# Kernel tuning notes

Measured on AMD Instinct MI355X. Metric: run time of the kernel, lower is better.

## Reference

```python
import jax, jax.numpy as jnp
import numpy as np
import math

B, Q_LEN, PAST, HID = 1, 1024, 3072, 4096
NH, NKV, HD = 32, 8, 128
KV_LEN = PAST + Q_LEN
ROPE_THETA = 10000.0


def setup_inputs() -> dict:
    key = jax.random.key(0)
    ks = jax.random.split(key, 8)
    s = 0.02
    hidden_states = jax.random.normal(ks[0], (B, Q_LEN, HID), jnp.float32)
    # additive causal mask with KV cache offset: query i attends keys j <= PAST + i
    i = jnp.arange(Q_LEN)[:, None]
    j = jnp.arange(KV_LEN)[None, :]
    attention_mask = jnp.where(j <= PAST + i, 0.0, -1e9).astype(jnp.float32)[None, None]
    position_ids = (jnp.arange(Q_LEN, dtype=jnp.int64) + PAST)[None, :]
    past_k = jax.random.normal(ks[1], (B, NKV, PAST, HD), jnp.float32)
    past_v = jax.random.normal(ks[2], (B, NKV, PAST, HD), jnp.float32)
    Wq = jax.random.normal(ks[3], (NH * HD, HID), jnp.float32) * s
    Wk = jax.random.normal(ks[4], (NKV * HD, HID), jnp.float32) * s
    Wv = jax.random.normal(ks[5], (NKV * HD, HID), jnp.float32) * s
    Wo = jax.random.normal(ks[6], (HID, NH * HD), jnp.float32) * s
    return {"hidden_states": hidden_states, "attention_mask": attention_mask,
            "position_ids": position_ids, "past_k": past_k, "past_v": past_v,
            "Wq": Wq, "Wk": Wk, "Wv": Wv, "Wo": Wo}


def _rope_tables(seq_len, head_dim, dtype):
    inv_freq = 1.0 / (ROPE_THETA ** (jnp.arange(0, head_dim, 2, dtype=jnp.float32) / head_dim))
    t = jnp.arange(seq_len, dtype=jnp.float32)
    freqs = jnp.outer(t, inv_freq)            # [seq, hd/2]
    emb = jnp.concatenate([freqs, freqs], -1)  # [seq, hd]
    return jnp.cos(emb).astype(dtype), jnp.sin(emb).astype(dtype)


def _rotate_half(x):
    x1, x2 = jnp.split(x, 2, axis=-1)
    return jnp.concatenate([-x2, x1], axis=-1)


def reference(hidden_states, attention_mask, position_ids, past_k, past_v, Wq, Wk, Wv, Wo):
    bsz, q_len, _ = hidden_states.shape
    q = (hidden_states @ Wq.T).reshape(bsz, q_len, NH, HD).transpose(0, 2, 1, 3)
    k = (hidden_states @ Wk.T).reshape(bsz, q_len, NKV, HD).transpose(0, 2, 1, 3)
    v = (hidden_states @ Wv.T).reshape(bsz, q_len, NKV, HD).transpose(0, 2, 1, 3)

    kv_seq_len = q_len + past_k.shape[2]
    cos_t, sin_t = _rope_tables(kv_seq_len, HD, q.dtype)
    cos = cos_t[position_ids][:, None]  # [b,1,q,hd]
    sin = sin_t[position_ids][:, None]
    q = q * cos + _rotate_half(q) * sin
    k = k * cos + _rotate_half(k) * sin

    k = jnp.concatenate([past_k, k], axis=2)  # [b,nkv,kv,hd]
    v = jnp.concatenate([past_v, v], axis=2)
    n_rep = NH // NKV
    k = jnp.repeat(k, n_rep, axis=1)  # GQA repeat_kv -> [b,nh,kv,hd]
    v = jnp.repeat(v, n_rep, axis=1)

    scores = jnp.einsum('bhqd,bhkd->bhqk', q, k) / math.sqrt(HD)
    scores = scores + attention_mask
    weights = jax.nn.softmax(scores.astype(jnp.float32), axis=-1).astype(q.dtype)
    attn = jnp.einsum('bhqk,bhkd->bhqd', weights, v)
    attn = attn.transpose(0, 2, 1, 3).reshape(bsz, q_len, NH * HD)
    return attn @ Wo.T
```

## Files before the change

### kernel.cpp

```cpp
#include <hip/hip_runtime.h>

#define QLEN 1024
#define PASTN 3072
#define KVLEN 4096
#define HIDN 4096
#define NHEAD 32
#define NKVH 8
#define HDIM 128
#define NQKVC 6144
#define PLANE ((size_t)QLEN * NQKVC)

typedef unsigned short u16;
typedef __bf16 bf16x8 __attribute__((ext_vector_type(8)));
typedef float f32x4 __attribute__((ext_vector_type(4)));
typedef float f32x16 __attribute__((ext_vector_type(16)));
typedef u16 us8 __attribute__((ext_vector_type(8)));
typedef u16 us4 __attribute__((ext_vector_type(4)));

__device__ __forceinline__ u16 f2bf(float x) {
  unsigned u = __builtin_bit_cast(unsigned, x);
  u += 0x7fffu + ((u >> 16) & 1u);
  return (u16)(u >> 16);
}
__device__ __forceinline__ float bf2f(u16 b) {
  return __builtin_bit_cast(float, (unsigned)b << 16);
}

#define GLL16(gp, lp) __builtin_amdgcn_global_load_lds( \
    (const __attribute__((address_space(1))) void*)(gp), \
    (__attribute__((address_space(3))) void*)(lp), 16, 0, 0)

__global__ __launch_bounds__(256) void cvt5_kernel(const float* __restrict__ hid,
                                                   const float* __restrict__ wq,
                                                   const float* __restrict__ wk,
                                                   const float* __restrict__ wv,
                                                   const float* __restrict__ woin,
                                                   u16* __restrict__ hb,
                                                   u16* __restrict__ wb,
                                                   u16* __restrict__ wob) {
  const int blk = blockIdx.x;
  const float* src;
  u16* dst;
  int off;
  if (blk < 4096)       { src = hid;  dst = hb;                       off = blk; }
  else if (blk < 20480) { src = wq;   dst = wb;                       off = blk - 4096; }
  else if (blk < 24576) { src = wk;   dst = wb + (size_t)4096 * HIDN; off = blk - 20480; }
  else if (blk < 28672) { src = wv;   dst = wb + (size_t)5120 * HIDN; off = blk - 24576; }
  else                  { src = woin; dst = wob;                      off = blk - 28672; }
  const int i = off * 1024 + threadIdx.x * 4;
  float4 f = *(const float4*)(src + i);
  ushort4 o = make_ushort4(f2bf(f.x), f2bf(f.y), f2bf(f.z), f2bf(f.w));
  *(ushort4*)(dst + i) = o;
}

__global__ __launch_bounds__(256) void gemm_bt_split(const u16* __restrict__ A,
                                                     const u16* __restrict__ B,
                                                     float* __restrict__ P,
                                                     int M, int N, int K, int Ks) {
  __shared__ u16 Alds[2][64 * 32];
  __shared__ u16 Blds[2][128 * 32];
  const int tid = threadIdx.x, wid = tid >> 6, lane = tid & 63;
  const int m0 = blockIdx.y * 64, n0 = blockIdx.x * 128;
  const int z = blockIdx.z;
  const u16* Az = A + (size_t)z * Ks;
  const u16* Bz = B + (size_t)z * Ks;
  float* Cz = P + (size_t)z * M * N;
  const int wm = (wid >> 1) * 32, wn = (wid & 1) * 64;
  const int l15 = lane & 15, l4 = lane >> 4;
  const int srow = lane >> 2, sp = lane & 3;
  f32x4 acc[2][4] = {};
  auto stage = [&](int buf, int kt) {
    {
      const int r = wid * 16 + srow;
      GLL16(Az + (size_t)(m0 + r) * K + kt + (sp ^ ((r >> 1) & 3)) * 8,
            &Alds[buf][wid * 512]);
    }
#pragma unroll
    for (int i = 0; i < 2; ++i) {
      const int c = wid * 2 + i;
      const int r = c * 16 + srow;
      GLL16(Bz + (size_t)(n0 + r) * K + kt + (sp ^ ((r >> 1) & 3)) * 8,
            &Blds[buf][c * 512]);
    }
  };
  stage(0, 0);
  __syncthreads();
  int cur = 0;
  for (int kt = 0; kt < Ks; kt += 32) {
    if (kt + 32 < Ks) stage(cur ^ 1, kt + 32);
    bf16x8 a[2], b[4];
#pragma unroll
    for (int i = 0; i < 2; ++i) {
      const int R = wm + i * 16 + l15;
      a[i] = *(const bf16x8*)&Alds[cur][R * 32 + (l4 ^ ((R >> 1) & 3)) * 8];
    }
#pragma unroll
    for (int j = 0; j < 4; ++j) {
      const int R = wn + j * 16 + l15;
      b[j] = *(const bf16x8*)&Blds[cur][R * 32 + (l4 ^ ((R >> 1) & 3)) * 8];
    }
#pragma unroll
    for (int i = 0; i < 2; ++i)
#pragma unroll
      for (int j = 0; j < 4; ++j)
        acc[i][j] = __builtin_amdgcn_mfma_f32_16x16x32_bf16(a[i], b[j], acc[i][j], 0, 0, 0);
    __syncthreads();
    cur ^= 1;
  }
#pragma unroll
  for (int i = 0; i < 2; ++i)
#pragma unroll
    for (int j = 0; j < 4; ++j) {
      int row = m0 + wm + i * 16 + l4 * 4;
      int col = n0 + wn + j * 16 + l15;
#pragma unroll
      for (int r = 0; r < 4; ++r) Cz[(size_t)(row + r) * N + col] = acc[i][j][r];
    }
}

__global__ __launch_bounds__(256) void comb2_f32(const float* __restrict__ P,
                                                 float* __restrict__ C, size_t MN) {
  const size_t i = ((size_t)blockIdx.x * 256 + threadIdx.x) * 4;
  f32x4 a = *(const f32x4*)(P + i);
  f32x4 b = *(const f32x4*)(P + MN + i);
  f32x4 o;
#pragma unroll
  for (int j = 0; j < 4; ++j) o[j] = a[j] + b[j];
  *(f32x4*)(C + i) = o;
}

__global__ __launch_bounds__(256) void rope_q_kernel(const float* __restrict__ g,
                                                     u16* __restrict__ qr) {
  const float SC = 0.12753102f;
  int idx = blockIdx.x * 256 + threadIdx.x;
  int i = idx & 63, h = (idx >> 6) & 31, r = idx >> 11;
  float freq = __expf(-(float)i * (9.210340371976184f / 64.f));
  float angle = (float)(PASTN + r) * freq;
  float sn, cs;
  sincosf(angle, &sn, &cs);
  const size_t base = (size_t)r * NQKVC + h * HDIM + i;
  float x1 = g[base] + g[base + PLANE];
  float x2 = g[base + 64] + g[base + 64 + PLANE];
  int ob = r * HIDN + h * HDIM + i;
  qr[ob] = f2bf((x1 * cs - x2 * sn) * SC);
  qr[ob + 64] = f2bf((x2 * cs + x1 * sn) * SC);
}

__global__ __launch_bounds__(256) void repack_k_kernel(const float* __restrict__ past_k,
                                                       const float* __restrict__ g,
                                                       u16* __restrict__ kb) {
  int idx = blockIdx.x * 256 + threadIdx.x;
  int d = idx & 127, kv = (idx >> 7) & 4095, hk = idx >> 19;
  float val;
  if (kv < PASTN) {
    val = past_k[((size_t)hk * PASTN + kv) * HDIM + d];
  } else {
    int r = kv - PASTN;
    const size_t b0 = (size_t)r * NQKVC + 4096 + hk * HDIM;
    float x = g[b0 + d] + g[b0 + d + PLANE];
    float xp = g[b0 + (d ^ 64)] + g[b0 + (d ^ 64) + PLANE];
    int i = d & 63;
    float freq = __expf(-(float)i * (9.210340371976184f / 64.f));
    float angle = (float)(PASTN + r) * freq;
    float sn, cs;
    sincosf(angle, &sn, &cs);
    val = (d < 64) ? (x * cs - xp * sn) : (x * cs + xp * sn);
  }
  kb[idx] = f2bf(val);
}

__global__ __launch_bounds__(256) void repack_vt_kernel(const float* __restrict__ past_v,
                                                        const float* __restrict__ g,
                                                        u16* __restrict__ vtb) {
  __shared__ u16 tile[32][136];
  int hk = blockIdx.y, kv0 = blockIdx.x * 32, tid = threadIdx.x;
  int j = tid >> 3, d0 = (tid & 7) * 16;
  if (kv0 < PASTN) {
    const float* src = past_v + ((size_t)hk * PASTN + kv0 + j) * HDIM + d0;
#pragma unroll
    for (int x = 0; x < 16; x += 4) {
      float4 f = *(const float4*)(src + x);
      tile[j][d0 + x] = f2bf(f.x);
      tile[j][d0 + x + 1] = f2bf(f.y);
      tile[j][d0 + x + 2] = f2bf(f.z);
      tile[j][d0 + x + 3] = f2bf(f.w);
    }
  } else {
    int r = kv0 - PASTN + j;
    const float* s0 = g + (size_t)r * NQKVC + 5120 + hk * HDIM + d0;
#pragma unroll
    for (int x = 0; x < 16; x += 4) {
      f32x4 a = *(const f32x4*)(s0 + x);
      f32x4 b = *(const f32x4*)(s0 + PLANE + x);
#pragma unroll
      for (int jj = 0; jj < 4; ++jj) tile[j][d0 + x + jj] = f2bf(a[jj] + b[jj]);
    }
  }
  __syncthreads();
  int d = tid >> 1, jb = (tid & 1) * 16;
  us8 o0, o1;
#pragma unroll
  for (int x = 0; x < 8; ++x) {
    o0[x] = tile[jb + x][d];
    o1[x] = tile[jb + 8 + x][d];
  }
  u16* dst = vtb + ((size_t)hk * HDIM + d) * KVLEN + kv0 + jb;
  *(us8*)dst = o0;
  *(us8*)(dst + 8) = o1;
}

__global__ __launch_bounds__(512) void attn_kernel(const u16* __restrict__ q,
                                                   const u16* __restrict__ kc,
                                                   const u16* __restrict__ vt,
                                                   float* __restrict__ opart,
                                                   float* __restrict__ mlbuf) {
  __shared__ u16 Klds[2][64 * 128];
  __shared__ u16 Vlds[2][128 * 64];
  const int tid = threadIdx.x, wid = tid >> 6, lane = tid & 63;
  const int l31 = lane & 31, hi = lane >> 5, l15 = lane & 15;
  const int h = blockIdx.y, hk = h >> 2;
  const int q0 = blockIdx.x * 256;
  const int z = blockIdx.z;
  const int pid = h * 4 + blockIdx.x;
  const int qrow = q0 + wid * 32 + l31;
  bf16x8 qf[8];
  {
    const u16* qp = q + (size_t)qrow * HIDN + h * HDIM + hi * 8;
#pragma unroll
    for (int dk = 0; dk < 8; ++dk) qf[dk] = *(const bf16x8*)(qp + dk * 16);
  }
  float m_run = -1e30f, l_run = 0.f;
  f32x16 oacc[4] = {};
  const u16* kbase = kc + (size_t)hk * KVLEN * HDIM;
  const u16* vbase = vt + (size_t)hk * HDIM * KVLEN;
  const int ntiles = (PASTN + q0 + 256) >> 6;
  const int half = ntiles >> 1;
  const int t0 = z ? half : 0, t1 = z ? ntiles : half;
  const int qpos = PASTN + qrow;
  auto stage = [&](int buf, int kv0) {
#pragma unroll
    for (int i = 0; i < 2; ++i) {
      const int w = wid * 2 + i;
      const int p = w * 4 + (lane >> 4);
      const int key = (p & 0x33) | ((p & 4) << 1) | ((p & 8) >> 1);
      const int sl = (lane & 15) ^ (p & 15);
      GLL16(kbase + (size_t)(kv0 + key) * HDIM + sl * 8, &Klds[buf][w * 512]);
    }
#pragma unroll
    for (int i = 0; i < 2; ++i) {
      const int w = wid * 2 + i;
      const int d = w * 8 + (lane >> 3);
      const int sl = (lane & 7) ^ ((lane >> 3) & 7);
      GLL16(vbase + (size_t)d * KVLEN + kv0 + sl * 8, &Vlds[buf][w * 512]);
    }
  };
  stage(0, t0 << 6);
  __syncthreads();
  int cur = 0;
  for (int t = t0; t < t1; ++t) {
    if (t + 1 < t1) stage(cur ^ 1, (t + 1) << 6);
    const int kv0 = t << 6;
    const u16* Kb = Klds[cur];
    const u16* Vb = Vlds[cur];
    f32x16 s[2] = {};
    __builtin_amdgcn_s_setprio(1);
#pragma unroll
    for (int tt = 0; tt < 2; ++tt)
#pragma unroll
      for (int dk = 0; dk < 8; ++dk) {
        const int idx = (tt * 32 + l31) * 128 + (((dk * 2 + hi) ^ l15) * 8);
        bf16x8 kf = *(const bf16x8*)&Kb[idx];
        s[tt] = __builtin_amdgcn_mfma_f32_32x32x16_bf16(kf, qf[dk], s[tt], 0, 0, 0);
      }
    __builtin_amdgcn_s_setprio(0);
    float pm = -1e30f;
    if (kv0 + 63 > PASTN + q0) {
#pragma unroll
      for (int tt = 0; tt < 2; ++tt)
#pragma unroll
        for (int reg = 0; reg < 16; ++reg) {
          const int key = kv0 + tt * 32 + (reg & 7) + 8 * hi + ((reg & 8) << 1);
          float v = s[tt][reg];
          if (key > qpos) v = -1e30f;
          s[tt][reg] = v;
          pm = fmaxf(pm, v);
        }
    } else {
#pragma unroll
      for (int tt = 0; tt < 2; ++tt)
#pragma unroll
        for (int reg = 0; reg < 16; ++reg) pm = fmaxf(pm, s[tt][reg]);
    }
    pm = fmaxf(pm, __shfl_xor(pm, 32));
    if (!__all(pm <= m_run)) {
      const float mn = fmaxf(m_run, pm);
      const float corr = exp2f(m_run - mn);
      m_run = mn;
      l_run *= corr;
#pragma unroll
      for (int db = 0; db < 4; ++db)
#pragma unroll
        for (int r = 0; r < 16; ++r) oacc[db][r] *= corr;
    }
    float rs = 0.f;
#pragma unroll
    for (int tt = 0; tt < 2; ++tt)
#pragma unroll
      for (int reg = 0; reg < 16; ++reg) {
        const float p = exp2f(s[tt][reg] - m_run);
        s[tt][reg] = p;
        rs += p;
      }
    rs += __shfl_xor(rs, 32);
    l_run += rs;
    __builtin_amdgcn_s_setprio(1);
#pragma unroll
    for (int kc2 = 0; kc2 < 4; ++kc2) {
      bf16x8 pa;
#pragma unroll
      for (int j = 0; j < 8; ++j) pa[j] = (__bf16)s[kc2 >> 1][(kc2 & 1) * 8 + j];
#pragma unroll
      for (int db = 0; db < 4; ++db) {
        const int idx = (db * 32 + l31) * 64 + (((kc2 * 2 + hi) ^ (l31 & 7)) * 8);
        bf16x8 vf = *(const bf16x8*)&Vb[idx];
        oacc[db] = __builtin_amdgcn_mfma_f32_32x32x16_bf16(vf, pa, oacc[db], 0, 0, 0);
      }
    }
    __builtin_amdgcn_s_setprio(0);
    __syncthreads();
    cur ^= 1;
  }
  const int orow = wid * 32 + l31;
  float* op = opart + ((size_t)(z * 128 + pid) * 256 + orow) * 128;
#pragma unroll
  for (int db = 0; db < 4; ++db)
#pragma unroll
    for (int g = 0; g < 4; ++g) {
      f32x4 w4;
#pragma unroll
      for (int j = 0; j < 4; ++j) w4[j] = oacc[db][g * 4 + j];
      *(f32x4*)&op[db * 32 + g * 8 + hi * 4] = w4;
    }
  if (hi == 0) {
    float* mlp = mlbuf + ((size_t)(z * 128 + pid) * 256 + orow) * 2;
    mlp[0] = m_run;
    mlp[1] = l_run;
  }
}

__global__ __launch_bounds__(256) void attn_combine(const float* __restrict__ opart,
                                                    const float* __restrict__ mlbuf,
                                                    u16* __restrict__ o) {
  const int pid = blockIdx.x;
  const int h = pid >> 2, qt = pid & 3;
  const int q2 = threadIdx.x >> 2, dc = (threadIdx.x & 3) * 32;
#pragma unroll
  for (int b = 0; b < 4; ++b) {
    const int q = b * 64 + q2;
    const float* ml0 = mlbuf + ((size_t)pid * 256 + q) * 2;
    const float* ml1 = mlbuf + ((size_t)(128 + pid) * 256 + q) * 2;
    const float m0 = ml0[0], l0 = ml0[1], m1 = ml1[0], l1 = ml1[1];
    const float m = fmaxf(m0, m1);
    const float w0 = exp2f(m0 - m), w1 = exp2f(m1 - m);
    const float inv = 1.f / (w0 * l0 + w1 * l1);
    const float* O0 = opart + ((size_t)pid * 256 + q) * 128 + dc;
    const float* O1 = opart + ((size_t)(128 + pid) * 256 + q) * 128 + dc;
    u16* dst = o + (size_t)(qt * 256 + q) * HIDN + h * HDIM + dc;
#pragma unroll
    for (int x = 0; x < 8; ++x) {
      f32x4 a = *(const f32x4*)(O0 + x * 4);
      f32x4 bb = *(const f32x4*)(O1 + x * 4);
      us4 w4;
#pragma unroll
      for (int j = 0; j < 4; ++j) w4[j] = f2bf((a[j] * w0 + bb[j] * w1) * inv);
      *(us4*)(dst + x * 4) = w4;
    }
  }
}

extern "C" void kernel_launch(void* const* d_in, const int* in_sizes, int n_in,
                              void* d_out, int out_size, void* d_ws, size_t ws_size,
                              hipStream_t stream) {
  (void)in_sizes; (void)n_in; (void)out_size; (void)ws_size;
  const float* hidden = (const float*)d_in[0];
  const float* past_k = (const float*)d_in[3];
  const float* past_v = (const float*)d_in[4];
  const float* Wq = (const float*)d_in[5];
  const float* Wk = (const float*)d_in[6];
  const float* Wv = (const float*)d_in[7];
  const float* Wo = (const float*)d_in[8];
  float* out = (float*)d_out;

  char* w = (char*)d_ws;
  u16* hiddenb = (u16*)w; w += (size_t)QLEN * HIDN * 2;
  u16* wqkv    = (u16*)w; w += (size_t)NQKVC * HIDN * 2;
  u16* wo      = (u16*)w; w += (size_t)HIDN * HIDN * 2;
  u16* qrope   = (u16*)w; w += (size_t)QLEN * HIDN * 2;
  u16* kbuf    = (u16*)w; w += (size_t)NKVH * KVLEN * HDIM * 2;
  u16* vtbuf   = (u16*)w; w += (size_t)NKVH * HDIM * KVLEN * 2;
  u16* attnb   = (u16*)w; w += (size_t)QLEN * HIDN * 2;
  float* gpart = (float*)w;
  float* opart = (float*)wqkv;
  float* mlbuf = opart + (size_t)2 * 128 * 256 * 128;
  const size_t MN2 = (size_t)QLEN * HIDN;

  cvt5_kernel<<<45056, 256, 0, stream>>>(hidden, Wq, Wk, Wv, Wo, hiddenb, wqkv, wo);

  gemm_bt_split<<<dim3(NQKVC / 128, QLEN / 64, 2), 256, 0, stream>>>(
      hiddenb, wqkv, gpart, QLEN, NQKVC, HIDN, HIDN / 2);

  rope_q_kernel<<<(QLEN * NHEAD * 64) / 256, 256, 0, stream>>>(gpart, qrope);
  repack_k_kernel<<<(NKVH * KVLEN * HDIM) / 256, 256, 0, stream>>>(past_k, gpart, kbuf);
  repack_vt_kernel<<<dim3(KVLEN / 32, NKVH), 256, 0, stream>>>(past_v, gpart, vtbuf);

  attn_kernel<<<dim3(QLEN / 256, NHEAD, 2), 512, 0, stream>>>(qrope, kbuf, vtbuf,
                                                              opart, mlbuf);
  attn_combine<<<128, 256, 0, stream>>>(opart, mlbuf, attnb);

  gemm_bt_split<<<dim3(HIDN / 128, QLEN / 64, 2), 256, 0, stream>>>(
      attnb, wo, gpart, QLEN, HIDN, HIDN, HIDN / 2);
  comb2_f32<<<(int)(MN2 / 1024), 256, 0, stream>>>(gpart, out, MN2);
}
```

Baseline: 331.9 us.

## Fuse fp32 weight-to-bf16 conversion into GEMM B-tile loads

Drops the separate pass that converted the Wq/Wk/Wv/Wo weights to bf16. The GEMMs now stage fp32 weight tiles straight into LDS with an XOR swizzle and convert them to bf16 in registers before the MFMA. This avoids writing and re-reading roughly 80MB of bf16 weights. In exchange, each GEMM reads fp32 weights (twice the bytes per tile), LDS use for B doubles, and every block repeats the conversion work.

```diff
diff --git a/kernel.cpp b/kernel.cpp
--- a/kernel.cpp
+++ b/kernel.cpp
@@ -30,57 +30,52 @@
     (const __attribute__((address_space(1))) void*)(gp), \
     (__attribute__((address_space(3))) void*)(lp), 16, 0, 0)
 
-__global__ __launch_bounds__(256) void cvt5_kernel(const float* __restrict__ hid,
-                                                   const float* __restrict__ wq,
-                                                   const float* __restrict__ wk,
-                                                   const float* __restrict__ wv,
-                                                   const float* __restrict__ woin,
-                                                   u16* __restrict__ hb,
-                                                   u16* __restrict__ wb,
-                                                   u16* __restrict__ wob) {
-  const int blk = blockIdx.x;
-  const float* src;
-  u16* dst;
-  int off;
-  if (blk < 4096)       { src = hid;  dst = hb;                       off = blk; }
-  else if (blk < 20480) { src = wq;   dst = wb;                       off = blk - 4096; }
-  else if (blk < 24576) { src = wk;   dst = wb + (size_t)4096 * HIDN; off = blk - 20480; }
-  else if (blk < 28672) { src = wv;   dst = wb + (size_t)5120 * HIDN; off = blk - 24576; }
-  else                  { src = woin; dst = wob;                      off = blk - 28672; }
-  const int i = off * 1024 + threadIdx.x * 4;
+__global__ __launch_bounds__(256) void cvt_kernel(const float* __restrict__ src,
+                                                  u16* __restrict__ dst, int n) {
+  int i = (blockIdx.x * 256 + threadIdx.x) * 4;
+  if (i >= n) return;
   float4 f = *(const float4*)(src + i);
   ushort4 o = make_ushort4(f2bf(f.x), f2bf(f.y), f2bf(f.z), f2bf(f.w));
   *(ushort4*)(dst + i) = o;
 }
 
-__global__ __launch_bounds__(256) void gemm_bt_split(const u16* __restrict__ A,
-                                                     const u16* __restrict__ B,
-                                                     float* __restrict__ P,
-                                                     int M, int N, int K, int Ks) {
+__global__ __launch_bounds__(256) void gemm_f32b_split(const u16* __restrict__ A,
+                                                       const float* __restrict__ b0,
+                                                       const float* __restrict__ b1,
+                                                       const float* __restrict__ b2,
+                                                       float* __restrict__ P,
+                                                       int M, int N, int K, int Ks,
+                                                       int S1, int S2) {
   __shared__ u16 Alds[2][64 * 32];
-  __shared__ u16 Blds[2][128 * 32];
+  __shared__ float Blds[2][128 * 32];
   const int tid = threadIdx.x, wid = tid >> 6, lane = tid & 63;
   const int m0 = blockIdx.y * 64, n0 = blockIdx.x * 128;
-  const int z = blockIdx.z;
-  const u16* Az = A + (size_t)z * Ks;
-  const u16* Bz = B + (size_t)z * Ks;
+  const int z = blockIdx.z, zoff = z * Ks;
+  const u16* Az = A + zoff;
+  const float* bsrc;
+  int rbase;
+  if (n0 < S1)      { bsrc = b0; rbase = n0; }
+  else if (n0 < S2) { bsrc = b1; rbase = n0 - S1; }
+  else              { bsrc = b2; rbase = n0 - S2; }
+  bsrc += zoff;
   float* Cz = P + (size_t)z * M * N;
   const int wm = (wid >> 1) * 32, wn = (wid & 1) * 64;
   const int l15 = lane & 15, l4 = lane >> 4;
-  const int srow = lane >> 2, sp = lane & 3;
+  const int srowA = lane >> 2, spA = lane & 3;
+  const int brow = lane >> 3, bch = lane & 7;
   f32x4 acc[2][4] = {};
   auto stage = [&](int buf, int kt) {
     {
-      const int r = wid * 16 + srow;
-      GLL16(Az + (size_t)(m0 + r) * K + kt + (sp ^ ((r >> 1) & 3)) * 8,
+      const int r = wid * 16 + srowA;
+      GLL16(Az + (size_t)(m0 + r) * K + kt + (spA ^ ((r >> 1) & 3)) * 8,
             &Alds[buf][wid * 512]);
     }
 #pragma unroll
-    for (int i = 0; i < 2; ++i) {
-      const int c = wid * 2 + i;
-      const int r = c * 16 + srow;
-      GLL16(Bz + (size_t)(n0 + r) * K + kt + (sp ^ ((r >> 1) & 3)) * 8,
-            &Blds[buf][c * 512]);
+    for (int i = 0; i < 4; ++i) {
+      const int w = wid * 4 + i;
+      const int r = w * 8 + brow;
+      const int c = bch ^ (r & 7);
+      GLL16(bsrc + (size_t)(rbase + r) * K + kt + c * 4, &Blds[buf][w * 256]);
     }
   };
   stage(0, 0);
@@ -97,7 +92,14 @@
 #pragma unroll
     for (int j = 0; j < 4; ++j) {
       const int R = wn + j * 16 + l15;
-      b[j] = *(const bf16x8*)&Blds[cur][R * 32 + (l4 ^ ((R >> 1) & 3)) * 8];
+      const int s0 = (2 * l4) ^ (R & 7), s1 = (2 * l4 + 1) ^ (R & 7);
+      f32x4 lo = *(const f32x4*)&Blds[cur][R * 32 + s0 * 4];
+      f32x4 hi = *(const f32x4*)&Blds[cur][R * 32 + s1 * 4];
+#pragma unroll
+      for (int jj = 0; jj < 4; ++jj) {
+        b[j][jj] = (__bf16)lo[jj];
+        b[j][4 + jj] = (__bf16)hi[jj];
+      }
     }
 #pragma unroll
     for (int i = 0; i < 2; ++i)
@@ -393,21 +395,19 @@
 
   char* w = (char*)d_ws;
   u16* hiddenb = (u16*)w; w += (size_t)QLEN * HIDN * 2;
-  u16* wqkv    = (u16*)w; w += (size_t)NQKVC * HIDN * 2;
-  u16* wo      = (u16*)w; w += (size_t)HIDN * HIDN * 2;
   u16* qrope   = (u16*)w; w += (size_t)QLEN * HIDN * 2;
   u16* kbuf    = (u16*)w; w += (size_t)NKVH * KVLEN * HDIM * 2;
   u16* vtbuf   = (u16*)w; w += (size_t)NKVH * HDIM * KVLEN * 2;
   u16* attnb   = (u16*)w; w += (size_t)QLEN * HIDN * 2;
-  float* gpart = (float*)w;
-  float* opart = (float*)wqkv;
-  float* mlbuf = opart + (size_t)2 * 128 * 256 * 128;
+  float* gpart = (float*)w; w += 2 * PLANE * sizeof(float);
+  float* opart = (float*)w; w += (size_t)2 * 128 * 256 * 128 * 4;
+  float* mlbuf = (float*)w;
   const size_t MN2 = (size_t)QLEN * HIDN;
 
-  cvt5_kernel<<<45056, 256, 0, stream>>>(hidden, Wq, Wk, Wv, Wo, hiddenb, wqkv, wo);
-
-  gemm_bt_split<<<dim3(NQKVC / 128, QLEN / 64, 2), 256, 0, stream>>>(
-      hiddenb, wqkv, gpart, QLEN, NQKVC, HIDN, HIDN / 2);
+  cvt_kernel<<<(QLEN * HIDN) / 1024, 256, 0, stream>>>(hidden, hiddenb, QLEN * HIDN);
+
+  gemm_f32b_split<<<dim3(NQKVC / 128, QLEN / 64, 2), 256, 0, stream>>>(
+      hiddenb, Wq, Wk, Wv, gpart, QLEN, NQKVC, HIDN, HIDN / 2, 4096, 5120);
 
   rope_q_kernel<<<(QLEN * NHEAD * 64) / 256, 256, 0, stream>>>(gpart, qrope);
   repack_k_kernel<<<(NKVH * KVLEN * HDIM) / 256, 256, 0, stream>>>(past_k, gpart, kbuf);
@@ -417,7 +417,7 @@
                                                               opart, mlbuf);
   attn_combine<<<128, 256, 0, stream>>>(opart, mlbuf, attnb);
 
-  gemm_bt_split<<<dim3(HIDN / 128, QLEN / 64, 2), 256, 0, stream>>>(
-      attnb, wo, gpart, QLEN, HIDN, HIDN, HIDN / 2);
+  gemm_f32b_split<<<dim3(HIDN / 128, QLEN / 64, 2), 256, 0, stream>>>(
+      attnb, Wo, Wo, Wo, gpart, QLEN, HIDN, HIDN, HIDN / 2, HIDN, 2 * HIDN);
   comb2_f32<<<(int)(MN2 / 1024), 256, 0, stream>>>(gpart, out, MN2);
 }
```

Result: slower. 365.1 us (+10.0%).
